# Kernel tuning notes

Hardware: AMD Instinct MI355X
Metric: run time of the kernel (lower is better)

Reference implementation:

```python
import jax, jax.numpy as jnp
import numpy as np

NUM_ATLAS = 100000
FD = 16
FS = 9  # fsize + 1
NV, NB = 65536, 8


def setup_inputs() -> dict:
    key = jax.random.key(0)
    k1, k2, k3 = jax.random.split(key, 3)
    x = jax.random.uniform(k1, (NV, NB, 2), minval=-1.0, maxval=1.0, dtype=jnp.float32)
    inds = jax.random.randint(k2, (NV, NB), 0, NUM_ATLAS)
    ft = jax.random.normal(k3, (NUM_ATLAS, FD, FS, FS), dtype=jnp.float32) * 0.1
    return {"x": x, "inds": inds, "ft": ft}


def reference(x, inds, ft):
    # Fused equivalent of: ft[inds] -> (Nv*Nb, fd, fs, fs) then
    # F.grid_sample(..., align_corners=True, padding_mode='border') at one point.
    # We index the 4 bilinear corners directly in the atlas (no big gather).
    fs = ft.shape[-1]
    # grid coords: x[...,0] -> width (last axis), x[...,1] -> height
    # align_corners=True: pix = (c + 1) / 2 * (fs - 1); border padding == clamp
    gx = jnp.clip((x[..., 0] + 1.0) * 0.5 * (fs - 1), 0.0, fs - 1.0)
    gy = jnp.clip((x[..., 1] + 1.0) * 0.5 * (fs - 1), 0.0, fs - 1.0)
    x0f = jnp.floor(gx)
    y0f = jnp.floor(gy)
    wx = (gx - x0f)[..., None]  # (Nv, Nb, 1)
    wy = (gy - y0f)[..., None]
    x0 = x0f.astype(jnp.int32)
    y0 = y0f.astype(jnp.int32)
    x1 = jnp.minimum(x0 + 1, fs - 1)
    y1 = jnp.minimum(y0 + 1, fs - 1)
    # advanced indexing with a slice in the middle -> (Nv, Nb, fd)
    v00 = ft[inds, :, y0, x0]
    v01 = ft[inds, :, y0, x1]
    v10 = ft[inds, :, y1, x0]
    v11 = ft[inds, :, y1, x1]
    top = v00 * (1.0 - wx) + v01 * wx
    bot = v10 * (1.0 - wx) + v11 * wx
    return top * (1.0 - wy) + bot * wy  # (Nv, Nb, fd)
```

## Files before the change

kernel.cpp:

```cpp
#include <hip/hip_runtime.h>


constexpr int FD = 16;
constexpr int FS = 9;
constexpr int ENTRY_FLOATS = FD * FS * FS;
constexpr int ENTRY_F4     = ENTRY_FLOATS / 4;
constexpr int NSAMP = 65536 * 8;
constexpr int NUM_ATLAS = 100000;
constexpr int BLOCK = 256;
constexpr int WAVES_PER_BLOCK = 4;

constexpr int SCAN_CHUNK = 1024;
constexpr int NUM_SCAN_BLOCKS = (NUM_ATLAS + SCAN_CHUNK - 1) / SCAN_CHUNK;
constexpr int PARTIALS_PAD = 128;


__global__ __launch_bounds__(BLOCK) void hist_kernel(const int* __restrict__ inds,
                                                     int* __restrict__ hist) {
    int i = blockIdx.x * BLOCK + threadIdx.x;
    if (i < NSAMP) atomicAdd(&hist[inds[i]], 1);
}

__global__ __launch_bounds__(BLOCK) void scanA_kernel(const int* __restrict__ hist,
                                                      int* __restrict__ offsets,
                                                      int* __restrict__ partials) {
    __shared__ int lds[BLOCK];
    int t = threadIdx.x;
    int base = blockIdx.x * SCAN_CHUNK + t * 4;
    int v[4];
    #pragma unroll
    for (int j = 0; j < 4; ++j) v[j] = (base + j < NUM_ATLAS) ? hist[base + j] : 0;
    int sum = v[0] + v[1] + v[2] + v[3];
    lds[t] = sum;
    __syncthreads();
    for (int off = 1; off < BLOCK; off <<= 1) {
        int add = (t >= off) ? lds[t - off] : 0;
        __syncthreads();
        lds[t] += add;
        __syncthreads();
    }
    int incl = lds[t];
    int excl = incl - sum;
    if (t == BLOCK - 1) partials[blockIdx.x] = incl;
    int run = excl;
    #pragma unroll
    for (int j = 0; j < 4; ++j) {
        if (base + j < NUM_ATLAS) offsets[base + j] = run;
        run += v[j];
    }
}

__global__ __launch_bounds__(128) void scanB_kernel(int* __restrict__ partials) {
    __shared__ int lds[128];
    int t = threadIdx.x;
    int v = (t < NUM_SCAN_BLOCKS) ? partials[t] : 0;
    lds[t] = v;
    __syncthreads();
    for (int off = 1; off < 128; off <<= 1) {
        int add = (t >= off) ? lds[t - off] : 0;
        __syncthreads();
        lds[t] += add;
        __syncthreads();
    }
    if (t < NUM_SCAN_BLOCKS) partials[t] = lds[t] - v;
}

__global__ __launch_bounds__(BLOCK) void scanC_kernel(int* __restrict__ offsets,
                                                      const int* __restrict__ partials) {
    int i = blockIdx.x * BLOCK + threadIdx.x;
    if (i < NUM_ATLAS) offsets[i] += partials[i / SCAN_CHUNK];
}

__global__ __launch_bounds__(BLOCK) void scatter_kernel(const int* __restrict__ inds,
                                                        int* __restrict__ offsets,
                                                        int* __restrict__ order) {
    int i = blockIdx.x * BLOCK + threadIdx.x;
    if (i < NSAMP) {
        int ind = inds[i];
        int pos = atomicAdd(&offsets[ind], 1);
        order[pos] = i;
    }
}

__global__ __launch_bounds__(BLOCK) void gather_kernel(
    const float2* __restrict__ x,
    const float*  __restrict__ ft,
    const int*    __restrict__ order,
    const int*    __restrict__ hist,
    const int*    __restrict__ seg_end,
    float*        __restrict__ out)
{
    __shared__ float4 tile[WAVES_PER_BLOCK][ENTRY_F4];
    const int wv   = threadIdx.x >> 6;
    const int lane = threadIdx.x & 63;
    const int e    = blockIdx.x * WAVES_PER_BLOCK + wv;

    const int end   = seg_end[e];
    const int cnt   = hist[e];
    const int start = end - cnt;

    if (cnt > 0) {
        const float4* src = (const float4*)(ft + (size_t)e * ENTRY_FLOATS);
        #pragma unroll
        for (int k = 0; k < 5; ++k)
            tile[wv][lane + 64 * k] = src[lane + 64 * k];
        if (lane < ENTRY_F4 - 320)
            tile[wv][320 + lane] = src[320 + lane];
    }
    __syncthreads();

    if (cnt == 0) return;

    const float* L  = (const float*)tile[wv];
    const int ch    = lane & 15;
    const int sub   = lane >> 4;
    const float fsm1 = (float)(FS - 1);

    for (int p = start + sub; p < end; p += 4) {
        int sid = order[p];
        float2 xy = x[sid];

        float gx = fminf(fmaxf((xy.x + 1.0f) * 0.5f * fsm1, 0.0f), fsm1);
        float gy = fminf(fmaxf((xy.y + 1.0f) * 0.5f * fsm1, 0.0f), fsm1);
        int x0 = min((int)gx, FS - 2);
        int y0 = min((int)gy, FS - 2);
        float wx = gx - (float)x0;
        float wy = gy - (float)y0;
        float w00 = (1.0f - wx) * (1.0f - wy);
        float w01 = wx * (1.0f - wy);
        float w10 = (1.0f - wx) * wy;
        float w11 = wx * wy;

        int base = ch * (FS * FS) + y0 * FS + x0;
        float r = L[base]          * w00 + L[base + 1]      * w01
                + L[base + FS]     * w10 + L[base + FS + 1] * w11;

        out[(size_t)sid * FD + ch] = r;
    }
}

extern "C" void kernel_launch(void* const* d_in, const int* in_sizes, int n_in,
                              void* d_out, int out_size, void* d_ws, size_t ws_size,
                              hipStream_t stream) {
    const float2* x    = (const float2*)d_in[0];
    const int*    inds = (const int*)d_in[1];
    const float*  ft   = (const float*)d_in[2];
    float*        out  = (float*)d_out;

    int* ws       = (int*)d_ws;
    int* hist     = ws;
    int* partials = hist + NUM_ATLAS;
    int* offsets  = partials + PARTIALS_PAD;
    int* order    = offsets + NUM_ATLAS;

    hipMemsetAsync(hist, 0, (size_t)NUM_ATLAS * sizeof(int), stream);

    hist_kernel<<<NSAMP / BLOCK, BLOCK, 0, stream>>>(inds, hist);
    scanA_kernel<<<NUM_SCAN_BLOCKS, BLOCK, 0, stream>>>(hist, offsets, partials);
    scanB_kernel<<<1, 128, 0, stream>>>(partials);
    scanC_kernel<<<(NUM_ATLAS + BLOCK - 1) / BLOCK, BLOCK, 0, stream>>>(offsets, partials);
    scatter_kernel<<<NSAMP / BLOCK, BLOCK, 0, stream>>>(inds, offsets, order);

    gather_kernel<<<NUM_ATLAS / WAVES_PER_BLOCK, BLOCK, 0, stream>>>(
        x, ft, order, hist, offsets, out);
}
```

Baseline: 735.5 us.

## Fuse scan passes, pre-sort coordinates in scatter, use direct global-to-LDS loads

Drops the single-block partials scan: each scanC block now reduces the chunk partials it needs itself. The scatter kernel also writes each sample's coordinates into sorted order, so the gather kernel reads them contiguously instead of through an indirect random load. The atlas tile is loaded with global_load_lds straight into shared memory, and waves with empty entries exit early instead of waiting at a block barrier. The cost is an extra sorted coordinate buffer that must be written and read, plus a per-wave wait that depends on the wave only reading its own tile.

```diff
diff --git a/kernel.cpp b/kernel.cpp
--- a/kernel.cpp
+++ b/kernel.cpp
@@ -50,42 +50,42 @@
     }
 }
 
-__global__ __launch_bounds__(128) void scanB_kernel(int* __restrict__ partials) {
-    __shared__ int lds[128];
+__global__ __launch_bounds__(BLOCK) void scanC_kernel(int* __restrict__ offsets,
+                                                      const int* __restrict__ partials) {
+    __shared__ int red[BLOCK];
     int t = threadIdx.x;
-    int v = (t < NUM_SCAN_BLOCKS) ? partials[t] : 0;
-    lds[t] = v;
+    int chunk = blockIdx.x >> 2;
+    int s = (t < chunk) ? partials[t] : 0;
+    red[t] = s;
     __syncthreads();
-    for (int off = 1; off < 128; off <<= 1) {
-        int add = (t >= off) ? lds[t - off] : 0;
-        __syncthreads();
-        lds[t] += add;
+    #pragma unroll
+    for (int off = BLOCK / 2; off > 0; off >>= 1) {
+        if (t < off) red[t] += red[t + off];
         __syncthreads();
     }
-    if (t < NUM_SCAN_BLOCKS) partials[t] = lds[t] - v;
-}
-
-__global__ __launch_bounds__(BLOCK) void scanC_kernel(int* __restrict__ offsets,
-                                                      const int* __restrict__ partials) {
-    int i = blockIdx.x * BLOCK + threadIdx.x;
-    if (i < NUM_ATLAS) offsets[i] += partials[i / SCAN_CHUNK];
+    int add = red[0];
+    int i = blockIdx.x * BLOCK + t;
+    if (i < NUM_ATLAS) offsets[i] += add;
 }
 
 __global__ __launch_bounds__(BLOCK) void scatter_kernel(const int* __restrict__ inds,
+                                                        const float2* __restrict__ x,
                                                         int* __restrict__ offsets,
-                                                        int* __restrict__ order) {
+                                                        int* __restrict__ order,
+                                                        float2* __restrict__ xs) {
     int i = blockIdx.x * BLOCK + threadIdx.x;
     if (i < NSAMP) {
         int ind = inds[i];
         int pos = atomicAdd(&offsets[ind], 1);
         order[pos] = i;
+        xs[pos]    = x[i];
     }
 }
 
 __global__ __launch_bounds__(BLOCK) void gather_kernel(
-    const float2* __restrict__ x,
     const float*  __restrict__ ft,
     const int*    __restrict__ order,
+    const float2* __restrict__ xs,
     const int*    __restrict__ hist,
     const int*    __restrict__ seg_end,
     float*        __restrict__ out)
@@ -95,21 +95,29 @@
     const int lane = threadIdx.x & 63;
     const int e    = blockIdx.x * WAVES_PER_BLOCK + wv;
 
-    const int end   = seg_end[e];
-    const int cnt   = hist[e];
+    const int end = seg_end[e];
+    const int cnt = hist[e];
+    if (cnt == 0) return;
     const int start = end - cnt;
 
-    if (cnt > 0) {
+    {
         const float4* src = (const float4*)(ft + (size_t)e * ENTRY_FLOATS);
         #pragma unroll
-        for (int k = 0; k < 5; ++k)
-            tile[wv][lane + 64 * k] = src[lane + 64 * k];
-        if (lane < ENTRY_F4 - 320)
-            tile[wv][320 + lane] = src[320 + lane];
+        for (int k = 0; k < 5; ++k) {
+            __builtin_amdgcn_global_load_lds(
+                (const __attribute__((address_space(1))) void*)(src + 64 * k + lane),
+                (__attribute__((address_space(3))) void*)(&tile[wv][64 * k]),
+                16, 0, 0);
+        }
+        if (lane < ENTRY_F4 - 320) {
+            __builtin_amdgcn_global_load_lds(
+                (const __attribute__((address_space(1))) void*)(src + 320 + lane),
+                (__attribute__((address_space(3))) void*)(&tile[wv][320]),
+                16, 0, 0);
+        }
     }
-    __syncthreads();
-
-    if (cnt == 0) return;
+    asm volatile("s_waitcnt vmcnt(0)" ::: "memory");
+    __builtin_amdgcn_sched_barrier(0);
 
     const float* L  = (const float*)tile[wv];
     const int ch    = lane & 15;
@@ -117,8 +125,8 @@
     const float fsm1 = (float)(FS - 1);
 
     for (int p = start + sub; p < end; p += 4) {
-        int sid = order[p];
-        float2 xy = x[sid];
+        int sid   = order[p];
+        float2 xy = xs[p];
 
         float gx = fminf(fmaxf((xy.x + 1.0f) * 0.5f * fsm1, 0.0f), fsm1);
         float gy = fminf(fmaxf((xy.y + 1.0f) * 0.5f * fsm1, 0.0f), fsm1);
@@ -147,20 +155,20 @@
     const float*  ft   = (const float*)d_in[2];
     float*        out  = (float*)d_out;
 
-    int* ws       = (int*)d_ws;
-    int* hist     = ws;
-    int* partials = hist + NUM_ATLAS;
-    int* offsets  = partials + PARTIALS_PAD;
-    int* order    = offsets + NUM_ATLAS;
+    int*    ws       = (int*)d_ws;
+    int*    hist     = ws;
+    int*    partials = hist + NUM_ATLAS;
+    int*    offsets  = partials + PARTIALS_PAD;
+    int*    order    = offsets + NUM_ATLAS;
+    float2* xs       = (float2*)(order + NSAMP);
 
     hipMemsetAsync(hist, 0, (size_t)NUM_ATLAS * sizeof(int), stream);
 
     hist_kernel<<<NSAMP / BLOCK, BLOCK, 0, stream>>>(inds, hist);
     scanA_kernel<<<NUM_SCAN_BLOCKS, BLOCK, 0, stream>>>(hist, offsets, partials);
-    scanB_kernel<<<1, 128, 0, stream>>>(partials);
     scanC_kernel<<<(NUM_ATLAS + BLOCK - 1) / BLOCK, BLOCK, 0, stream>>>(offsets, partials);
-    scatter_kernel<<<NSAMP / BLOCK, BLOCK, 0, stream>>>(inds, offsets, order);
+    scatter_kernel<<<NSAMP / BLOCK, BLOCK, 0, stream>>>(inds, x, offsets, order, xs);
 
     gather_kernel<<<NUM_ATLAS / WAVES_PER_BLOCK, BLOCK, 0, stream>>>(
-        x, ft, order, hist, offsets, out);
+        ft, order, xs, hist, offsets, out);
 }
```

Measured after the change: 741.1 us. Within noise of the previous version (+0.8%).
